# Kernel tuning notes

Hardware: AMD Instinct MI355X
Metric: run time of the kernel (lower is better)

## Reference

```python
import jax, jax.numpy as jnp
import numpy as np

B, SQ, SK, D_MODEL, H, D = 2, 2048, 2048, 1024, 16, 64


def setup_inputs() -> dict:
    key = jax.random.key(0)
    ks = jax.random.split(key, 10)
    s = 1.0 / np.sqrt(D_MODEL)
    return {
        "x": jax.random.normal(ks[0], (B, SK, D_MODEL), jnp.float32),
        "x2": jax.random.normal(ks[1], (B, SQ, D_MODEL), jnp.float32),
        "Wq": jax.random.normal(ks[2], (H, D_MODEL, D), jnp.float32) * s,
        "bq": jax.random.normal(ks[3], (H, D), jnp.float32) * s,
        "Wk": jax.random.normal(ks[4], (H, D_MODEL, D), jnp.float32) * s,
        "bk": jax.random.normal(ks[5], (H, D), jnp.float32) * s,
        "Wv": jax.random.normal(ks[6], (H, D_MODEL, D), jnp.float32) * s,
        "bv": jax.random.normal(ks[7], (H, D), jnp.float32) * s,
        "Wo": jax.random.normal(ks[8], (D_MODEL, D_MODEL), jnp.float32) * s,
        "bo": jax.random.normal(ks[9], (D_MODEL,), jnp.float32) * s,
    }


def reference(x, x2, Wq, bq, Wk, bk, Wv, bv, Wo, bo):
    # Batched per-head projections (fuses the Python per-head loop).
    # q: [B, H, SQ, D]; k,v: [B, H, SK, D]
    q = jnp.einsum("bsm,hmd->bhsd", x2, Wq) + bq[None, :, None, :]
    k = jnp.einsum("bsm,hmd->bhsd", x, Wk) + bk[None, :, None, :]
    v = jnp.einsum("bsm,hmd->bhsd", x, Wv) + bv[None, :, None, :]
    scale = 1.0 / jnp.sqrt(jnp.asarray(D, q.dtype))
    scores = jnp.einsum("bhqd,bhkd->bhqk", q, k) * scale  # [B,H,SQ,SK]
    attn = jax.nn.softmax(scores, axis=-1)
    o = jnp.einsum("bhqk,bhkd->bhqd", attn, v)  # [B,H,SQ,D]
    # concat heads along feature dim (head-major order matches torch.cat)
    o = o.transpose(0, 2, 1, 3).reshape(B, SQ, H * D)
    # final projection; dropout is identity in eval mode
    return o @ Wo.T + bo
```

## Files before the change

kernel.cpp:

```cpp
#include <hip/hip_runtime.h>
#include <math.h>

#define B_   2
#define SQ_  2048
#define SK_  2048
#define DM_  1024
#define H_   16
#define D_   64

typedef __attribute__((ext_vector_type(8))) short bf16x8;
typedef __attribute__((ext_vector_type(4))) float f32x4;
typedef unsigned int u32;

__device__ __forceinline__ short f2bf(float f) {
    union { float f; unsigned u; } v; v.f = f;
    unsigned r = v.u + 0x7FFFu + ((v.u >> 16) & 1u);
    return (short)(r >> 16);
}
__device__ __forceinline__ u32 pk2bf(float x, float y) {
    union { float f; u32 u; } a, b; a.f = x; b.f = y;
    return ((a.u + 0x8000u) >> 16) | ((b.u + 0x8000u) & 0xFFFF0000u);
}

__device__ __forceinline__ void gll16(const void* g, void* l) {
    __builtin_amdgcn_global_load_lds(
        (const __attribute__((address_space(1))) u32*)g,
        (__attribute__((address_space(3))) u32*)l, 16, 0, 0);
}

__global__ __launch_bounds__(256) void prep_kernel(
    const float* __restrict__ Wq, const float* __restrict__ Wk,
    const float* __restrict__ Wv, const float* __restrict__ Wo,
    const float* __restrict__ x,  const float* __restrict__ x2,
    short* __restrict__ WqT, short* __restrict__ WkT,
    short* __restrict__ WvT, short* __restrict__ Wob,
    short* __restrict__ xb,  short* __restrict__ x2b)
{
    const int t = threadIdx.x;
    const int z = blockIdx.z;
    if (z >= 3) {
        const float* src = (z == 3) ? Wo : (z == 4) ? x : x2;
        short* dst       = (z == 3) ? Wob : (z == 4) ? xb : x2b;
        int nloop = (z == 3) ? 4 : 16;
        int bid = blockIdx.y * 16 + blockIdx.x;
        #pragma unroll 4
        for (int j = 0; j < nloop; j++) {
            int i = bid * (nloop * 256) + j * 256 + t;
            float4 v = ((const float4*)src)[i];
            short4 s;
            s.x = f2bf(v.x); s.y = f2bf(v.y); s.z = f2bf(v.z); s.w = f2bf(v.w);
            ((short4*)dst)[i] = s;
        }
        return;
    }
    const float* W = (z == 0) ? Wq : (z == 1) ? Wk : Wv;
    short* WT      = (z == 0) ? WqT : (z == 1) ? WkT : WvT;
    const int h  = blockIdx.y;
    const int m0 = blockIdx.x * 64;
    __shared__ short Ls[64][68];

    #pragma unroll
    for (int it = 0; it < 4; it++) {
        int lin = it * 256 + t;
        int m = lin >> 4, d4 = lin & 15;
        float4 v = *(const float4*)&W[((long)h * DM_ + m0 + m) * D_ + d4 * 4];
        short4 s;
        s.x = f2bf(v.x); s.y = f2bf(v.y); s.z = f2bf(v.z); s.w = f2bf(v.w);
        *(short4*)&Ls[m][d4 * 4] = s;
    }
    __syncthreads();
    #pragma unroll
    for (int it = 0; it < 2; it++) {
        int d = (t >> 3) + it * 32, scol = t & 7;
        bf16x8 vv;
        #pragma unroll
        for (int j = 0; j < 8; j++) vv[j] = Ls[scol * 8 + j][d];
        *(bf16x8*)&WT[((long)h * 64 + d) * DM_ + m0 + scol * 8] = vv;
    }
}

template <int MODE>
__device__ __forceinline__ void gemm_core(
    const short* __restrict__ A, const short* __restrict__ Bw,
    const float* __restrict__ bias, void* __restrict__ outp,
    int r0, int n0, float oscale)
{
    __shared__ short As[128 * 64];
    __shared__ short Bs[128 * 64];

    const int t    = threadIdx.x;
    const int w    = t >> 6;
    const int ln   = t & 63;
    const int l15  = ln & 15;
    const int quad = ln >> 4;
    const int wr   = w >> 1;
    const int wc   = w & 1;

    f32x4 acc[4][4];
    #pragma unroll
    for (int i = 0; i < 4; i++)
        #pragma unroll
        for (int j = 0; j < 4; j++) acc[i][j] = (f32x4){0.f, 0.f, 0.f, 0.f};

    const int srow = ln >> 3;
    const int sc   = (ln & 7) ^ srow;
    const int rsw  = l15 & 7;

    for (int k0 = 0; k0 < 1024; k0 += 64) {
        __syncthreads();
        #pragma unroll
        for (int j = 0; j < 4; j++) {
            int q   = w * 4 + j;
            int row = q * 8 + srow;
            gll16(A  + ((long)(r0 + row) << 10) + k0 + sc * 8, As + q * 512);
            gll16(Bw + ((long)(n0 + row) << 10) + k0 + sc * 8, Bs + q * 512);
        }
        __syncthreads();
        #pragma unroll
        for (int kh = 0; kh < 2; kh++) {
            bf16x8 af[4], bfr[4];
            #pragma unroll
            for (int i = 0; i < 4; i++) {
                int ra = wr * 64 + i * 16 + l15;
                int rb = wc * 64 + i * 16 + l15;
                int pc = ((kh * 4 + quad) ^ rsw) * 8;
                af[i]  = *(const bf16x8*)&As[ra * 64 + pc];
                bfr[i] = *(const bf16x8*)&Bs[rb * 64 + pc];
            }
            #pragma unroll
            for (int i = 0; i < 4; i++)
                #pragma unroll
                for (int j = 0; j < 4; j++)
                    acc[i][j] = __builtin_amdgcn_mfma_f32_16x16x32_bf16(
                        af[i], bfr[j], acc[i][j], 0, 0, 0);
        }
    }

    #pragma unroll
    for (int j = 0; j < 4; j++) {
        int col = n0 + wc * 64 + j * 16 + l15;
        float bv = bias[col];
        if (MODE == 2) {
            int hh = col >> 6, dd = col & 63;
            #pragma unroll
            for (int i = 0; i < 4; i++) {
                int rowb = r0 + wr * 64 + i * 16 + quad * 4;
                int bb = rowb >> 11, ss = rowb & 2047;
                int sl = ss & 63;
                int sp = (ss & ~63) | (sl & 35) | ((sl & 12) << 1) | ((sl & 16) >> 2);
                short4 sv;
                sv.x = f2bf(acc[i][j][0] + bv);
                sv.y = f2bf(acc[i][j][1] + bv);
                sv.z = f2bf(acc[i][j][2] + bv);
                sv.w = f2bf(acc[i][j][3] + bv);
                *(short4*)&((short*)outp)[
                    ((long)(((bb << 4) + hh) * 64 + dd) << 11) + sp] = sv;
            }
        } else {
            #pragma unroll
            for (int i = 0; i < 4; i++) {
                int rowb = r0 + wr * 64 + i * 16 + quad * 4;
                #pragma unroll
                for (int r = 0; r < 4; r++) {
                    float v = (acc[i][j][r] + bv) * oscale;
                    if (MODE == 0)
                        ((short*)outp)[(long)(rowb + r) * 1024 + col] = f2bf(v);
                    else
                        ((float*)outp)[(long)(rowb + r) * 1024 + col] = v;
                }
            }
        }
    }
}

#define QSCALE 0.180336880977f

__global__ __launch_bounds__(256) void gemm_qkv_kernel(
    const short* __restrict__ x2b, const short* __restrict__ xb,
    const short* __restrict__ WqT, const short* __restrict__ WkT,
    const short* __restrict__ WvT,
    const float* __restrict__ bq, const float* __restrict__ bk,
    const float* __restrict__ bv,
    short* __restrict__ Qb, short* __restrict__ Kb, short* __restrict__ VT)
{
    const int z = blockIdx.z;
    if (z == 0) {
        gemm_core<0>(x2b, WqT, bq, Qb, blockIdx.x * 128, blockIdx.y * 128, QSCALE);
    } else if (z == 1) {
        gemm_core<0>(xb, WkT, bk, Kb, blockIdx.x * 128, blockIdx.y * 128, 1.0f);
    } else {
        gemm_core<2>(xb, WvT, bv, VT, blockIdx.x * 128, blockIdx.y * 128, 1.0f);
    }
}

__global__ __launch_bounds__(256) void gemm_out_kernel(
    const short* __restrict__ A, const short* __restrict__ Bw,
    const float* __restrict__ bias, float* __restrict__ outp)
{
    __shared__ short As[64 * 64];
    __shared__ short Bs[128 * 64];

    const int r0   = blockIdx.x * 64;
    const int n0   = blockIdx.y * 128;
    const int t    = threadIdx.x;
    const int w    = t >> 6;
    const int ln   = t & 63;
    const int l15  = ln & 15;
    const int quad = ln >> 4;
    const int wr   = w >> 1;
    const int wc   = w & 1;

    f32x4 acc[2][4];
    #pragma unroll
    for (int i = 0; i < 2; i++)
        #pragma unroll
        for (int j = 0; j < 4; j++) acc[i][j] = (f32x4){0.f, 0.f, 0.f, 0.f};

    const int srow = ln >> 3;
    const int sc   = (ln & 7) ^ srow;
    const int rsw  = l15 & 7;

    for (int k0 = 0; k0 < 1024; k0 += 64) {
        __syncthreads();
        #pragma unroll
        for (int j = 0; j < 6; j++) {
            int q = w * 6 + j;
            if (q < 8) {
                int row = q * 8 + srow;
                gll16(A + ((long)(r0 + row) << 10) + k0 + sc * 8, As + q * 512);
            } else {
                int qb = q - 8;
                int row = qb * 8 + srow;
                gll16(Bw + ((long)(n0 + row) << 10) + k0 + sc * 8, Bs + qb * 512);
            }
        }
        __syncthreads();
        #pragma unroll
        for (int kh = 0; kh < 2; kh++) {
            int pc = ((kh * 4 + quad) ^ rsw) * 8;
            bf16x8 af[2], bfr[4];
            #pragma unroll
            for (int i = 0; i < 2; i++)
                af[i] = *(const bf16x8*)&As[(wr * 32 + i * 16 + l15) * 64 + pc];
            #pragma unroll
            for (int j = 0; j < 4; j++)
                bfr[j] = *(const bf16x8*)&Bs[(wc * 64 + j * 16 + l15) * 64 + pc];
            #pragma unroll
            for (int i = 0; i < 2; i++)
                #pragma unroll
                for (int j = 0; j < 4; j++)
                    acc[i][j] = __builtin_amdgcn_mfma_f32_16x16x32_bf16(
                        af[i], bfr[j], acc[i][j], 0, 0, 0);
        }
    }

    #pragma unroll
    for (int j = 0; j < 4; j++) {
        int col = n0 + wc * 64 + j * 16 + l15;
        float bv = bias[col];
        #pragma unroll
        for (int i = 0; i < 2; i++) {
            int rowb = r0 + wr * 32 + i * 16 + quad * 4;
            #pragma unroll
            for (int r = 0; r < 4; r++)
                outp[(long)(rowb + r) * 1024 + col] = acc[i][j][r] + bv;
        }
    }
}

__global__ __launch_bounds__(256) void flash_kernel(
    const short* __restrict__ Q, const short* __restrict__ K,
    const short* __restrict__ VT, short* __restrict__ O)
{
    const int t    = threadIdx.x;
    const int wave = t >> 6;
    const int ln   = t & 63;
    const int l15  = ln & 15;
    const int quad = ln >> 4;
    const int bh = blockIdx.y;
    const int b  = bh >> 4;
    const int h  = bh & 15;
    const int q0 = blockIdx.x * 128;
    const int wq = q0 + wave * 32;

    __shared__ short Ks[2][2][64 * 64];
    __shared__ short Vs[2][2][64 * 64];

    const int srow = ln >> 3;
    const int sc   = (ln & 7) ^ srow;
    const int rsw  = l15 & 7;

    bf16x8 aQ0[2], aQ1[2];
    #pragma unroll
    for (int qg = 0; qg < 2; qg++) {
        const short* Qp = Q + ((long)(b * SQ_ + wq + qg * 16 + l15)) * 1024
                            + h * 64 + quad * 8;
        aQ0[qg] = *(const bf16x8*)(Qp);
        aQ1[qg] = *(const bf16x8*)(Qp + 32);
    }

    bf16x8 ones;
    #pragma unroll
    for (int j = 0; j < 8; j++) ones[j] = (short)0x3F80;

    f32x4 o_acc[2][4];
    f32x4 l_acc[2];
    #pragma unroll
    for (int qg = 0; qg < 2; qg++) {
        l_acc[qg] = (f32x4){0.f, 0.f, 0.f, 0.f};
        #pragma unroll
        for (int i = 0; i < 4; i++) o_acc[qg][i] = (f32x4){0.f, 0.f, 0.f, 0.f};
    }

    const short* Kbase = K  + ((long)b * SK_) * 1024 + h * 64;
    const short* Vbase = VT + (long)bh * D_ * SK_;
    const int qqa = wave * 2, qqb = wave * 2 + 1;
    const int rowa = qqa * 8 + srow, rowb_ = qqb * 8 + srow;

    #define STAGE(bufp, half, kbase)                                            \
        gll16(Kbase + (long)((kbase) + rowa)  * 1024 + sc * 8,                  \
              &Ks[bufp][half][qqa * 512]);                                      \
        gll16(Kbase + (long)((kbase) + rowb_) * 1024 + sc * 8,                  \
              &Ks[bufp][half][qqb * 512]);                                      \
        gll16(Vbase + (long)rowa  * 2048 + (kbase) + sc * 8,                    \
              &Vs[bufp][half][qqa * 512]);                                      \
        gll16(Vbase + (long)rowb_ * 2048 + (kbase) + sc * 8,                    \
              &Vs[bufp][half][qqb * 512]);

    STAGE(0, 0, 0)
    STAGE(0, 1, 64)

    int cur = 0;
    for (int k0 = 0; k0 < SK_; k0 += 128) {
        __syncthreads();
        if (k0 + 128 < SK_) {
            int nx = cur ^ 1;
            STAGE(nx, 0, k0 + 128)
            STAGE(nx, 1, k0 + 192)
        }

        #pragma unroll
        for (int half = 0; half < 2; half++) {
            const short* Kst = &Ks[cur][half][0];
            const short* Vst = &Vs[cur][half][0];

            u32 pw[2][8];
            #pragma unroll
            for (int kt = 0; kt < 4; kt++) {
                const short* kr = &Kst[(kt * 16 + l15) * 64];
                bf16x8 ka0 = *(const bf16x8*)&kr[((quad    ) ^ rsw) * 8];
                bf16x8 ka1 = *(const bf16x8*)&kr[((quad + 4) ^ rsw) * 8];
                #pragma unroll
                for (int qg = 0; qg < 2; qg++) {
                    f32x4 z = (f32x4){0.f, 0.f, 0.f, 0.f};
                    z = __builtin_amdgcn_mfma_f32_16x16x32_bf16(ka0, aQ0[qg], z, 0, 0, 0);
                    z = __builtin_amdgcn_mfma_f32_16x16x32_bf16(ka1, aQ1[qg], z, 0, 0, 0);
                    float p0 = __builtin_amdgcn_exp2f(z[0]);
                    float p1 = __builtin_amdgcn_exp2f(z[1]);
                    float p2 = __builtin_amdgcn_exp2f(z[2]);
                    float p3 = __builtin_amdgcn_exp2f(z[3]);
                    pw[qg][kt * 2    ] = pk2bf(p0, p1);
                    pw[qg][kt * 2 + 1] = pk2bf(p2, p3);
                }
            }

            bf16x8 aP0[2], aP1[2];
            #pragma unroll
            for (int qg = 0; qg < 2; qg++) {
                union { bf16x8 v; u32 w[4]; } u0, u1;
                u0.w[0] = pw[qg][0]; u0.w[1] = pw[qg][1];
                u0.w[2] = pw[qg][2]; u0.w[3] = pw[qg][3];
                u1.w[0] = pw[qg][4]; u1.w[1] = pw[qg][5];
                u1.w[2] = pw[qg][6]; u1.w[3] = pw[qg][7];
                aP0[qg] = u0.v; aP1[qg] = u1.v;
            }

            __builtin_amdgcn_s_setprio(1);
            #pragma unroll
            for (int qg = 0; qg < 2; qg++) {
                l_acc[qg] = __builtin_amdgcn_mfma_f32_16x16x32_bf16(aP0[qg], ones, l_acc[qg], 0, 0, 0);
                l_acc[qg] = __builtin_amdgcn_mfma_f32_16x16x32_bf16(aP1[qg], ones, l_acc[qg], 0, 0, 0);
            }
            #pragma unroll
            for (int dt = 0; dt < 4; dt++) {
                const short* vr = &Vst[(dt * 16 + l15) * 64];
                bf16x8 bv0 = *(const bf16x8*)&vr[((quad    ) ^ rsw) * 8];
                bf16x8 bv1 = *(const bf16x8*)&vr[((quad + 4) ^ rsw) * 8];
                #pragma unroll
                for (int qg = 0; qg < 2; qg++) {
                    o_acc[qg][dt] = __builtin_amdgcn_mfma_f32_16x16x32_bf16(aP0[qg], bv0, o_acc[qg][dt], 0, 0, 0);
                    o_acc[qg][dt] = __builtin_amdgcn_mfma_f32_16x16x32_bf16(aP1[qg], bv1, o_acc[qg][dt], 0, 0, 0);
                }
            }
            __builtin_amdgcn_s_setprio(0);
        }
        cur ^= 1;
    }
    #undef STAGE

    #pragma unroll
    for (int qg = 0; qg < 2; qg++) {
        #pragma unroll
        for (int r = 0; r < 4; r++) {
            float inv = 1.0f / l_acc[qg][r];
            long row = (long)b * SQ_ + wq + qg * 16 + quad * 4 + r;
            short* Op = O + row * 1024 + h * 64 + l15;
            #pragma unroll
            for (int dt = 0; dt < 4; dt++)
                Op[dt * 16] = f2bf(o_acc[qg][dt][r] * inv);
        }
    }
}

extern "C" void kernel_launch(void* const* d_in, const int* in_sizes, int n_in,
                              void* d_out, int out_size, void* d_ws, size_t ws_size,
                              hipStream_t stream) {
    const float* x  = (const float*)d_in[0];
    const float* x2 = (const float*)d_in[1];
    const float* Wq = (const float*)d_in[2];
    const float* bq = (const float*)d_in[3];
    const float* Wk = (const float*)d_in[4];
    const float* bk = (const float*)d_in[5];
    const float* Wv = (const float*)d_in[6];
    const float* bv = (const float*)d_in[7];
    const float* Wo = (const float*)d_in[8];
    const float* bo = (const float*)d_in[9];
    float* out = (float*)d_out;

    const size_t nAct = (size_t)B_ * SK_ * DM_;
    const size_t nW   = (size_t)DM_ * DM_;
    short* bufA = (short*)d_ws;
    short* bufB = bufA + nAct;
    short* Qb   = bufB + nAct;
    short* Kb   = Qb + nAct;
    short* VTws = Kb + nAct;
    short* WqT  = VTws + nAct;
    short* WkT  = WqT + nW;
    short* WvT  = WkT + nW;
    short* Wob  = WvT + nW;

    prep_kernel<<<dim3(16, 16, 6), 256, 0, stream>>>(
        Wq, Wk, Wv, Wo, x, x2, WqT, WkT, WvT, Wob, bufA, bufB);

    gemm_qkv_kernel<<<dim3(32, 8, 3), 256, 0, stream>>>(
        bufB, bufA, WqT, WkT, WvT, bq, bk, bv, Qb, Kb, VTws);

    flash_kernel<<<dim3(16, 32), 256, 0, stream>>>(Qb, Kb, VTws, bufB);
    gemm_out_kernel<<<dim3(64, 8), 256, 0, stream>>>(bufB, Wob, bo, out);
}
```

Before: 211.5 us.

## Software-pipeline QK^T MFMA with exp2 across the two K halves of each tile

Restructures the attention inner loop so the QK^T MFMAs for the second 64-key half are interleaved with the exp2/pack work for the first half, and the exp2 for the second half is interleaved with the PV MFMAs of the first half. This aims to overlap transcendental VALU work with matrix-core work inside a wave. It also replaces the shift/mask bf16 packing with a single byte-permute instruction. Keeping more score fragments live raises register pressure, which could reduce occupancy.

```diff
diff --git a/kernel.cpp b/kernel.cpp
--- a/kernel.cpp
+++ b/kernel.cpp
@@ -20,6 +20,10 @@
 __device__ __forceinline__ u32 pk2bf(float x, float y) {
     union { float f; u32 u; } a, b; a.f = x; b.f = y;
     return ((a.u + 0x8000u) >> 16) | ((b.u + 0x8000u) & 0xFFFF0000u);
+}
+__device__ __forceinline__ u32 pkbf_rh(float x, float y) {
+    union { float f; u32 u; } a, b; a.f = x; b.f = y;
+    return __builtin_amdgcn_perm(b.u + 0x8000u, a.u + 0x8000u, 0x07060302u);
 }
 
 __device__ __forceinline__ void gll16(const void* g, void* l) {
@@ -303,13 +307,15 @@
     #pragma unroll
     for (int j = 0; j < 8; j++) ones[j] = (short)0x3F80;
 
+    const f32x4 fz = (f32x4){0.f, 0.f, 0.f, 0.f};
+
     f32x4 o_acc[2][4];
     f32x4 l_acc[2];
     #pragma unroll
     for (int qg = 0; qg < 2; qg++) {
-        l_acc[qg] = (f32x4){0.f, 0.f, 0.f, 0.f};
-        #pragma unroll
-        for (int i = 0; i < 4; i++) o_acc[qg][i] = (f32x4){0.f, 0.f, 0.f, 0.f};
+        l_acc[qg] = fz;
+        #pragma unroll
+        for (int i = 0; i < 4; i++) o_acc[qg][i] = fz;
     }
 
     const short* Kbase = K  + ((long)b * SK_) * 1024 + h * 64;
@@ -338,62 +344,109 @@
             STAGE(nx, 0, k0 + 128)
             STAGE(nx, 1, k0 + 192)
         }
-
-        #pragma unroll
-        for (int half = 0; half < 2; half++) {
-            const short* Kst = &Ks[cur][half][0];
-            const short* Vst = &Vs[cur][half][0];
-
-            u32 pw[2][8];
-            #pragma unroll
-            for (int kt = 0; kt < 4; kt++) {
-                const short* kr = &Kst[(kt * 16 + l15) * 64];
-                bf16x8 ka0 = *(const bf16x8*)&kr[((quad    ) ^ rsw) * 8];
-                bf16x8 ka1 = *(const bf16x8*)&kr[((quad + 4) ^ rsw) * 8];
-                #pragma unroll
-                for (int qg = 0; qg < 2; qg++) {
-                    f32x4 z = (f32x4){0.f, 0.f, 0.f, 0.f};
-                    z = __builtin_amdgcn_mfma_f32_16x16x32_bf16(ka0, aQ0[qg], z, 0, 0, 0);
-                    z = __builtin_amdgcn_mfma_f32_16x16x32_bf16(ka1, aQ1[qg], z, 0, 0, 0);
-                    float p0 = __builtin_amdgcn_exp2f(z[0]);
-                    float p1 = __builtin_amdgcn_exp2f(z[1]);
-                    float p2 = __builtin_amdgcn_exp2f(z[2]);
-                    float p3 = __builtin_amdgcn_exp2f(z[3]);
-                    pw[qg][kt * 2    ] = pk2bf(p0, p1);
-                    pw[qg][kt * 2 + 1] = pk2bf(p2, p3);
-                }
-            }
-
-            bf16x8 aP0[2], aP1[2];
+        const short* K0 = &Ks[cur][0][0];
+        const short* K1 = &Ks[cur][1][0];
+        const short* V0 = &Vs[cur][0][0];
+        const short* V1 = &Vs[cur][1][0];
+
+        f32x4 zA[2][4], zB[2][4];
+        u32 pwA[2][8], pwB[2][8];
+
+        #pragma unroll
+        for (int kt = 0; kt < 4; kt++) {
+            const short* kr = &K0[(kt * 16 + l15) * 64];
+            bf16x8 ka0 = *(const bf16x8*)&kr[((quad    ) ^ rsw) * 8];
+            bf16x8 ka1 = *(const bf16x8*)&kr[((quad + 4) ^ rsw) * 8];
             #pragma unroll
             for (int qg = 0; qg < 2; qg++) {
-                union { bf16x8 v; u32 w[4]; } u0, u1;
-                u0.w[0] = pw[qg][0]; u0.w[1] = pw[qg][1];
-                u0.w[2] = pw[qg][2]; u0.w[3] = pw[qg][3];
-                u1.w[0] = pw[qg][4]; u1.w[1] = pw[qg][5];
-                u1.w[2] = pw[qg][6]; u1.w[3] = pw[qg][7];
-                aP0[qg] = u0.v; aP1[qg] = u1.v;
-            }
-
-            __builtin_amdgcn_s_setprio(1);
+                f32x4 z = __builtin_amdgcn_mfma_f32_16x16x32_bf16(ka0, aQ0[qg], fz, 0, 0, 0);
+                z = __builtin_amdgcn_mfma_f32_16x16x32_bf16(ka1, aQ1[qg], z, 0, 0, 0);
+                zA[qg][kt] = z;
+            }
+        }
+
+        #pragma unroll
+        for (int kt = 0; kt < 4; kt++) {
+            const short* kr = &K1[(kt * 16 + l15) * 64];
+            bf16x8 ka0 = *(const bf16x8*)&kr[((quad    ) ^ rsw) * 8];
+            bf16x8 ka1 = *(const bf16x8*)&kr[((quad + 4) ^ rsw) * 8];
             #pragma unroll
             for (int qg = 0; qg < 2; qg++) {
-                l_acc[qg] = __builtin_amdgcn_mfma_f32_16x16x32_bf16(aP0[qg], ones, l_acc[qg], 0, 0, 0);
-                l_acc[qg] = __builtin_amdgcn_mfma_f32_16x16x32_bf16(aP1[qg], ones, l_acc[qg], 0, 0, 0);
-            }
-            #pragma unroll
-            for (int dt = 0; dt < 4; dt++) {
-                const short* vr = &Vst[(dt * 16 + l15) * 64];
-                bf16x8 bv0 = *(const bf16x8*)&vr[((quad    ) ^ rsw) * 8];
-                bf16x8 bv1 = *(const bf16x8*)&vr[((quad + 4) ^ rsw) * 8];
-                #pragma unroll
-                for (int qg = 0; qg < 2; qg++) {
-                    o_acc[qg][dt] = __builtin_amdgcn_mfma_f32_16x16x32_bf16(aP0[qg], bv0, o_acc[qg][dt], 0, 0, 0);
-                    o_acc[qg][dt] = __builtin_amdgcn_mfma_f32_16x16x32_bf16(aP1[qg], bv1, o_acc[qg][dt], 0, 0, 0);
-                }
-            }
-            __builtin_amdgcn_s_setprio(0);
-        }
+                f32x4 z = __builtin_amdgcn_mfma_f32_16x16x32_bf16(ka0, aQ0[qg], fz, 0, 0, 0);
+                z = __builtin_amdgcn_mfma_f32_16x16x32_bf16(ka1, aQ1[qg], z, 0, 0, 0);
+                zB[qg][kt] = z;
+            }
+            #pragma unroll
+            for (int qg = 0; qg < 2; qg++) {
+                f32x4 s = zA[qg][kt];
+                pwA[qg][kt * 2    ] = pkbf_rh(__builtin_amdgcn_exp2f(s[0]),
+                                              __builtin_amdgcn_exp2f(s[1]));
+                pwA[qg][kt * 2 + 1] = pkbf_rh(__builtin_amdgcn_exp2f(s[2]),
+                                              __builtin_amdgcn_exp2f(s[3]));
+            }
+        }
+
+        bf16x8 aP0A[2], aP1A[2];
+        #pragma unroll
+        for (int qg = 0; qg < 2; qg++) {
+            union { bf16x8 v; u32 w[4]; } u0, u1;
+            u0.w[0] = pwA[qg][0]; u0.w[1] = pwA[qg][1];
+            u0.w[2] = pwA[qg][2]; u0.w[3] = pwA[qg][3];
+            u1.w[0] = pwA[qg][4]; u1.w[1] = pwA[qg][5];
+            u1.w[2] = pwA[qg][6]; u1.w[3] = pwA[qg][7];
+            aP0A[qg] = u0.v; aP1A[qg] = u1.v;
+            l_acc[qg] = __builtin_amdgcn_mfma_f32_16x16x32_bf16(aP0A[qg], ones, l_acc[qg], 0, 0, 0);
+            l_acc[qg] = __builtin_amdgcn_mfma_f32_16x16x32_bf16(aP1A[qg], ones, l_acc[qg], 0, 0, 0);
+        }
+
+        #pragma unroll
+        for (int dt = 0; dt < 4; dt++) {
+            const short* vr = &V0[(dt * 16 + l15) * 64];
+            bf16x8 bv0 = *(const bf16x8*)&vr[((quad    ) ^ rsw) * 8];
+            bf16x8 bv1 = *(const bf16x8*)&vr[((quad + 4) ^ rsw) * 8];
+            #pragma unroll
+            for (int qg = 0; qg < 2; qg++) {
+                o_acc[qg][dt] = __builtin_amdgcn_mfma_f32_16x16x32_bf16(aP0A[qg], bv0, o_acc[qg][dt], 0, 0, 0);
+                o_acc[qg][dt] = __builtin_amdgcn_mfma_f32_16x16x32_bf16(aP1A[qg], bv1, o_acc[qg][dt], 0, 0, 0);
+            }
+            #pragma unroll
+            for (int qg = 0; qg < 2; qg++) {
+                f32x4 s = zB[qg][dt];
+                pwB[qg][dt * 2    ] = pkbf_rh(__builtin_amdgcn_exp2f(s[0]),
+                                              __builtin_amdgcn_exp2f(s[1]));
+                pwB[qg][dt * 2 + 1] = pkbf_rh(__builtin_amdgcn_exp2f(s[2]),
+                                              __builtin_amdgcn_exp2f(s[3]));
+            }
+        }
+
+        bf16x8 aP0B[2], aP1B[2];
+        #pragma unroll
+        for (int qg = 0; qg < 2; qg++) {
+            union { bf16x8 v; u32 w[4]; } u0, u1;
+            u0.w[0] = pwB[qg][0]; u0.w[1] = pwB[qg][1];
+            u0.w[2] = pwB[qg][2]; u0.w[3] = pwB[qg][3];
+            u1.w[0] = pwB[qg][4]; u1.w[1] = pwB[qg][5];
+            u1.w[2] = pwB[qg][6]; u1.w[3] = pwB[qg][7];
+            aP0B[qg] = u0.v; aP1B[qg] = u1.v;
+        }
+        __builtin_amdgcn_s_setprio(1);
+        #pragma unroll
+        for (int qg = 0; qg < 2; qg++) {
+            l_acc[qg] = __builtin_amdgcn_mfma_f32_16x16x32_bf16(aP0B[qg], ones, l_acc[qg], 0, 0, 0);
+            l_acc[qg] = __builtin_amdgcn_mfma_f32_16x16x32_bf16(aP1B[qg], ones, l_acc[qg], 0, 0, 0);
+        }
+        #pragma unroll
+        for (int dt = 0; dt < 4; dt++) {
+            const short* vr = &V1[(dt * 16 + l15) * 64];
+            bf16x8 bv0 = *(const bf16x8*)&vr[((quad    ) ^ rsw) * 8];
+            bf16x8 bv1 = *(const bf16x8*)&vr[((quad + 4) ^ rsw) * 8];
+            #pragma unroll
+            for (int qg = 0; qg < 2; qg++) {
+                o_acc[qg][dt] = __builtin_amdgcn_mfma_f32_16x16x32_bf16(aP0B[qg], bv0, o_acc[qg][dt], 0, 0, 0);
+                o_acc[qg][dt] = __builtin_amdgcn_mfma_f32_16x16x32_bf16(aP1B[qg], bv1, o_acc[qg][dt], 0, 0, 0);
+            }
+        }
+        __builtin_amdgcn_s_setprio(0);
         cur ^= 1;
     }
     #undef STAGE
```

Result: no change. 210.4 us (-0.5%).
